# Performance work log

Hardware: AMD Instinct MI355X
Metric: run time of the kernel (lower is better)

Reference implementation:

```python
import jax, jax.numpy as jnp
import numpy as np

# Static problem configuration
NUM_GRAPHS = 64
NODES_PER_GRAPH = 2048          # divisible by OUT_H
NODE_EMB_DIM = 256              # divisible by OUT_W
COND_EMB_DIM = 64
OUT_H, OUT_W = 16, 8            # AdaptiveAvgPool2d output -> pooled dim H*W = 128
MLP_H = 256
BN_EPS = 1e-5


def setup_inputs() -> dict:
    key = jax.random.key(0)
    ks = jax.random.split(key, 8)
    N = NUM_GRAPHS * NODES_PER_GRAPH
    x = jax.random.normal(ks[0], (N, NODE_EMB_DIM), dtype=jnp.float32)
    # equal contiguous segments: node i belongs to graph i // NODES_PER_GRAPH
    batch = jnp.repeat(jnp.arange(NUM_GRAPHS, dtype=jnp.int64), NODES_PER_GRAPH)
    conditioner_z_ref = jax.random.normal(ks[1], (N, COND_EMB_DIM), dtype=jnp.float32)
    mlp_in = COND_EMB_DIM + OUT_H * OUT_W
    W1 = jax.random.normal(ks[2], (mlp_in, MLP_H), dtype=jnp.float32) / np.sqrt(mlp_in)
    b1 = jnp.zeros((MLP_H,), dtype=jnp.float32)
    gamma = jnp.ones((MLP_H,), dtype=jnp.float32)
    beta = jnp.zeros((MLP_H,), dtype=jnp.float32)
    W2 = jax.random.normal(ks[3], (MLP_H, 3), dtype=jnp.float32) / np.sqrt(MLP_H)
    b2 = jnp.zeros((3,), dtype=jnp.float32)
    return {"x": x, "batch": batch, "conditioner_z_ref": conditioner_z_ref,
            "W1": W1, "b1": b1, "gamma": gamma, "beta": beta, "W2": W2, "b2": b2}


def _adaptive_pool(x):
    # x: [N_total, D] with equal contiguous segments of NODES_PER_GRAPH rows per graph.
    # AdaptiveAvgPool2d((OUT_H, OUT_W)) on each [n, D] "image"; since n % OUT_H == 0
    # and D % OUT_W == 0 the adaptive bins are uniform -> exact reshape-mean.
    B = x.shape[0] // NODES_PER_GRAPH
    xg = x.reshape(B, OUT_H, NODES_PER_GRAPH // OUT_H, OUT_W, NODE_EMB_DIM // OUT_W)
    pooled = xg.mean(axis=(2, 4))                 # [B, OUT_H, OUT_W]
    return pooled.reshape(B, OUT_H * OUT_W)       # [B, H*W]


def reference(x, batch, conditioner_z_ref, W1, b1, gamma, beta, W2, b2):
    batch_pooled = _adaptive_pool(x)                          # [B, H*W]
    gathered = batch_pooled[batch]                            # [N, H*W]
    h = jnp.concatenate([conditioner_z_ref, gathered], axis=1)  # [N, cond + H*W]
    # Linear -> BatchNorm1d (training-mode batch stats, biased var) -> GELU (exact)
    h = h @ W1 + b1                                           # [N, MLP_H]
    mean = h.mean(axis=0)
    var = h.var(axis=0)
    h = (h - mean) * jax.lax.rsqrt(var + BN_EPS) * gamma + beta
    h = jax.nn.gelu(h, approximate=False)
    return h @ W2 + b2                                        # [N, 3]
```

## Files before the change

kernel.cpp:

```cpp
#include <hip/hip_runtime.h>
#include <math.h>

#define NG    64
#define NPG   2048
#define NTOT  (NG*NPG)
#define ZD    64
#define PD    128
#define MH    256

typedef __attribute__((ext_vector_type(8))) short bf16x8;
typedef __attribute__((ext_vector_type(4))) float f32x4;

__device__ __forceinline__ unsigned short f2bf(float f){
  unsigned u = __float_as_uint(f);
  unsigned r = u + 0x7FFFu + ((u >> 16) & 1u);
  return (unsigned short)(r >> 16);
}
__device__ __forceinline__ float bf2f(unsigned short s){
  return __uint_as_float(((unsigned)s) << 16);
}
__device__ __forceinline__ float gelu_f(float x){
  float u = x * x;
  float a = fmaf(0.044715f, u, 1.0f);
  float e = __builtin_amdgcn_exp2f(-2.3022083f * x * a);
  return x * __builtin_amdgcn_rcpf(1.0f + e);
}

__launch_bounds__(256)
__global__ void k1_pool_zstat(const float* __restrict__ x, const float* __restrict__ z,
                              float* __restrict__ pooled, float* __restrict__ St,
                              float* __restrict__ C){
  __shared__ __align__(16) unsigned short s_zt[64 * 264];
  __shared__ float s_cred[4096];
  int tid = threadIdx.x;

  if (blockIdx.x >= 256){
    int bi = blockIdx.x - 256;
    int b  = bi >> 4;
    int oh = bi & 15;
    int c4 = tid & 63;
    int rq = tid >> 6;
    const float4* x4 = (const float4*)x;
    size_t base = (size_t)(b * NPG + oh * 128) * 64;
    float4 acc = make_float4(0.f, 0.f, 0.f, 0.f);
    #pragma unroll 8
    for (int i = 0; i < 32; i++){
      float4 v = x4[base + (size_t)(rq + i * 4) * 64 + c4];
      acc.x += v.x; acc.y += v.y; acc.z += v.z; acc.w += v.w;
    }
    s_cred[tid] = acc.x + acc.y + acc.z + acc.w;
    __syncthreads();
    if (tid < 8){
      float s = 0.f;
      #pragma unroll
      for (int w = 0; w < 4; w++)
        #pragma unroll
        for (int j = 0; j < 8; j++)
          s += s_cred[w * 64 + tid * 8 + j];
      pooled[b * PD + oh * 8 + tid] = s * (1.0f / 4096.0f);
    }
    return;
  }

  int blk = blockIdx.x;
  int g = blk >> 2, q4 = blk & 3;
  int lane = tid & 63, wave = tid >> 6;
  int col = lane & 15, quad = lane >> 4;
  const float4* z4 = (const float4*)z + ((size_t)g * 2048 + q4 * 512) * 16;
  int d4 = col;
  int mg = quad;

  f32x4 acc[4][4];
  #pragma unroll
  for (int a = 0; a < 4; a++)
    #pragma unroll
    for (int b = 0; b < 4; b++) acc[a][b] = (f32x4)(0.f);
  float s0 = 0.f, s1 = 0.f, s2 = 0.f, s3 = 0.f;

  for (int ch = 0; ch < 2; ch++){
    #pragma unroll
    for (int rd = 0; rd < 4; rd++){
      int m0 = rd * 64 + wave * 16 + mg * 4;
      const float4* src = z4 + ch * 4096 + m0 * 16 + d4;
      float4 v0 = src[0];
      float4 v1 = src[16];
      float4 v2 = src[32];
      float4 v3 = src[48];
      s0 += v0.x + v1.x + v2.x + v3.x;
      s1 += v0.y + v1.y + v2.y + v3.y;
      s2 += v0.z + v1.z + v2.z + v3.z;
      s3 += v0.w + v1.w + v2.w + v3.w;
      int slot = m0 >> 3;
      int sub  = m0 & 4;
      int d0 = d4 * 4;
      {
        int d = d0 + 0; int ss = slot ^ ((d >> 3) & 7);
        ushort4 w = make_ushort4(f2bf(v0.x), f2bf(v1.x), f2bf(v2.x), f2bf(v3.x));
        *(ushort4*)&s_zt[d * 264 + ss * 8 + sub] = w;
      }
      {
        int d = d0 + 1; int ss = slot ^ ((d >> 3) & 7);
        ushort4 w = make_ushort4(f2bf(v0.y), f2bf(v1.y), f2bf(v2.y), f2bf(v3.y));
        *(ushort4*)&s_zt[d * 264 + ss * 8 + sub] = w;
      }
      {
        int d = d0 + 2; int ss = slot ^ ((d >> 3) & 7);
        ushort4 w = make_ushort4(f2bf(v0.z), f2bf(v1.z), f2bf(v2.z), f2bf(v3.z));
        *(ushort4*)&s_zt[d * 264 + ss * 8 + sub] = w;
      }
      {
        int d = d0 + 3; int ss = slot ^ ((d >> 3) & 7);
        ushort4 w = make_ushort4(f2bf(v0.w), f2bf(v1.w), f2bf(v2.w), f2bf(v3.w));
        *(ushort4*)&s_zt[d * 264 + ss * 8 + sub] = w;
      }
    }
    __syncthreads();
    #pragma unroll
    for (int ks = 0; ks < 2; ks++){
      bf16x8 fr[4];
      #pragma unroll
      for (int t = 0; t < 4; t++){
        int row = t * 16 + col;
        int ss  = (wave * 8 + ks * 4 + quad) ^ ((row >> 3) & 7);
        fr[t] = *(const bf16x8*)&s_zt[row * 264 + ss * 8];
      }
      #pragma unroll
      for (int mt = 0; mt < 4; mt++)
        #pragma unroll
        for (int nt = 0; nt < 4; nt++)
          acc[mt][nt] = __builtin_amdgcn_mfma_f32_16x16x32_bf16(fr[mt], fr[nt], acc[mt][nt], 0, 0, 0);
    }
    __syncthreads();
  }

  s0 += __shfl_xor(s0, 16); s0 += __shfl_xor(s0, 32);
  s1 += __shfl_xor(s1, 16); s1 += __shfl_xor(s1, 32);
  s2 += __shfl_xor(s2, 16); s2 += __shfl_xor(s2, 32);
  s3 += __shfl_xor(s3, 16); s3 += __shfl_xor(s3, 32);
  if (quad == 0){
    atomicAdd(&St[(d4 * 4 + 0) * 64 + g], s0);
    atomicAdd(&St[(d4 * 4 + 1) * 64 + g], s1);
    atomicAdd(&St[(d4 * 4 + 2) * 64 + g], s2);
    atomicAdd(&St[(d4 * 4 + 3) * 64 + g], s3);
  }

  #pragma unroll
  for (int w = 0; w < 4; w++){
    if (wave == w){
      #pragma unroll
      for (int mt = 0; mt < 4; mt++)
        #pragma unroll
        for (int nt = 0; nt < 4; nt++)
          #pragma unroll
          for (int r = 0; r < 4; r++){
            int p = mt * 16 + quad * 4 + r;
            int qc = nt * 16 + col;
            if (w == 0) s_cred[p * 64 + qc]  = acc[mt][nt][r];
            else        s_cred[p * 64 + qc] += acc[mt][nt][r];
          }
    }
    __syncthreads();
  }
  for (int f = tid; f < 4096; f += 256)
    atomicAdd(&C[f], s_cred[f]);
}

__launch_bounds__(256)
__global__ void k2_stats(const float* __restrict__ pooled, const float* __restrict__ W1,
                         const float* __restrict__ b1, const float* __restrict__ gamma,
                         const float* __restrict__ beta, const float* __restrict__ C,
                         const float* __restrict__ St, float* __restrict__ Aj,
                         float* __restrict__ cprime, unsigned short* __restrict__ Wbf){
  __shared__ float pl[64 * 129];
  int tid = threadIdx.x;
  int jc = tid >> 6, lane = tid & 63;
  int j = blockIdx.x * 4 + jc;

  Wbf[(size_t)j * 64 + lane] = f2bf(W1[(size_t)lane * 256 + j]);

  for (int idx = tid; idx < 8192; idx += 256)
    pl[(idx >> 7) * 129 + (idx & 127)] = pooled[idx];
  __syncthreads();

  float g = b1[j];
  #pragma unroll 8
  for (int k = 0; k < 128; k++)
    g = fmaf(pl[lane * 129 + k], W1[(size_t)(ZD + k) * MH + j], g);

  float wl = W1[(size_t)lane * MH + j];
  float t1 = 0.f, t2 = 0.f;
  #pragma unroll
  for (int q = 0; q < 64; q++){
    float wq = __uint_as_float(__builtin_amdgcn_readlane(__float_as_uint(wl), q));
    t1 = fmaf(C [q * 64 + lane], wq, t1);
    t2 = fmaf(St[q * 64 + lane], wq, t2);
  }
  float v_wcw = wl * t1;
  float v_gs  = g * t2;
  float v_s   = t2;
  float v_g   = g;
  float v_g2  = g * g;
  #pragma unroll
  for (int off = 32; off; off >>= 1){
    v_wcw += __shfl_xor(v_wcw, off);
    v_gs  += __shfl_xor(v_gs , off);
    v_s   += __shfl_xor(v_s  , off);
    v_g   += __shfl_xor(v_g  , off);
    v_g2  += __shfl_xor(v_g2 , off);
  }
  const float invN = 1.0f / (float)NTOT;
  float mean = v_s * invN + v_g * (1.0f / 64.0f);
  float eh2  = v_wcw * invN + 2.0f * invN * v_gs + v_g2 * (1.0f / 64.0f);
  float var  = eh2 - mean * mean;
  float aj = gamma[j] * rsqrtf(var + 1e-5f);
  if (lane == 0) Aj[j] = aj;
  cprime[lane * MH + j] = fmaf(aj, g, beta[j] - aj * mean);
}

__launch_bounds__(256, 4)
__global__ void final_kernel(const float* __restrict__ z, const unsigned short* __restrict__ Wbf,
                             const float* __restrict__ Aj, const float* __restrict__ cp,
                             const float* __restrict__ W2, const float* __restrict__ b2,
                             float* __restrict__ out){
  __shared__ __align__(16) unsigned short zt[64 * 136];
  __shared__ float slab[4 * 192];
  int tid = threadIdx.x;
  int u  = blockIdx.x;
  int n0 = u * 64;
  int g  = u >> 5;

  const float4* z4 = (const float4*)z + (size_t)n0 * 16;
  #pragma unroll
  for (int i = 0; i < 4; i++){
    int idx = tid + i * 256;
    int m = idx >> 4, d4 = idx & 15;
    float4 v = z4[idx];
    ushort4 h, l;
    h.x = f2bf(v.x); l.x = f2bf(v.x - bf2f(h.x));
    h.y = f2bf(v.y); l.y = f2bf(v.y - bf2f(h.y));
    h.z = f2bf(v.z); l.z = f2bf(v.z - bf2f(h.z));
    h.w = f2bf(v.w); l.w = f2bf(v.w - bf2f(h.w));
    *(ushort4*)&zt[m * 136 + d4 * 4]      = h;
    *(ushort4*)&zt[m * 136 + 64 + d4 * 4] = l;
  }
  __syncthreads();

  int lane = tid & 63, wave = tid >> 6;
  int col = lane & 15, quad = lane >> 4;
  int nbase = wave * 64;

  f32x4 acc[4][4];
  #pragma unroll
  for (int mt = 0; mt < 4; mt++)
    #pragma unroll
    for (int nt = 0; nt < 4; nt++) acc[mt][nt] = (f32x4)(0.f);

  #pragma unroll
  for (int ks = 0; ks < 4; ks++){
    int k0 = ks * 32;
    bf16x8 af[4];
    #pragma unroll
    for (int mt = 0; mt < 4; mt++)
      af[mt] = *(const bf16x8*)&zt[(mt * 16 + col) * 136 + k0 + quad * 8];
    #pragma unroll
    for (int nt = 0; nt < 4; nt++){
      bf16x8 bv = *(const bf16x8*)&Wbf[(size_t)(nbase + nt * 16 + col) * 64 + (ks & 1) * 32 + quad * 8];
      #pragma unroll
      for (int mt = 0; mt < 4; mt++)
        acc[mt][nt] = __builtin_amdgcn_mfma_f32_16x16x32_bf16(af[mt], bv, acc[mt][nt], 0, 0, 0);
    }
  }

  float aj[4], cj[4], w2a[4], w2b[4], w2c[4];
  #pragma unroll
  for (int nt = 0; nt < 4; nt++){
    int j = nbase + nt * 16 + col;
    aj[nt] = Aj[j];
    cj[nt] = cp[g * MH + j];
    w2a[nt] = W2[j * 3 + 0];
    w2b[nt] = W2[j * 3 + 1];
    w2c[nt] = W2[j * 3 + 2];
  }

  #pragma unroll
  for (int mt = 0; mt < 4; mt++){
    #pragma unroll
    for (int r = 0; r < 4; r++){
      float o0 = 0.f, o1 = 0.f, o2 = 0.f;
      #pragma unroll
      for (int nt = 0; nt < 4; nt++){
        float h  = fmaf(aj[nt], acc[mt][nt][r], cj[nt]);
        float ge = gelu_f(h);
        o0 = fmaf(ge, w2a[nt], o0);
        o1 = fmaf(ge, w2b[nt], o1);
        o2 = fmaf(ge, w2c[nt], o2);
      }
      #pragma unroll
      for (int off = 8; off; off >>= 1){
        o0 += __shfl_xor(o0, off);
        o1 += __shfl_xor(o1, off);
        o2 += __shfl_xor(o2, off);
      }
      if (col == 0){
        int node = mt * 16 + quad * 4 + r;
        slab[wave * 192 + node * 3 + 0] = o0;
        slab[wave * 192 + node * 3 + 1] = o1;
        slab[wave * 192 + node * 3 + 2] = o2;
      }
    }
  }
  __syncthreads();
  if (tid < 192){
    float b2v = b2[tid % 3];
    out[(size_t)u * 192 + tid] = slab[tid] + slab[192 + tid] + slab[384 + tid] + slab[576 + tid] + b2v;
  }
}

extern "C" void kernel_launch(void* const* d_in, const int* in_sizes, int n_in,
                              void* d_out, int out_size, void* d_ws, size_t ws_size,
                              hipStream_t stream){
  (void)in_sizes; (void)n_in; (void)out_size; (void)ws_size;
  const float* x     = (const float*)d_in[0];
  const float* z     = (const float*)d_in[2];
  const float* W1    = (const float*)d_in[3];
  const float* b1    = (const float*)d_in[4];
  const float* gamma = (const float*)d_in[5];
  const float* beta  = (const float*)d_in[6];
  const float* W2    = (const float*)d_in[7];
  const float* b2    = (const float*)d_in[8];
  float* out = (float*)d_out;

  float* W = (float*)d_ws;
  float* pooled = W;
  float* St     = W + 8192;
  float* C      = W + 12288;
  float* Aj     = W + 16384;
  float* CP     = W + 16640;
  unsigned short* Wbf = (unsigned short*)(W + 33024);

  hipMemsetAsync((char*)d_ws + 8192 * 4, 0, 8192 * 4, stream);

  k1_pool_zstat<<<dim3(1280), dim3(256), 0, stream>>>(x, z, pooled, St, C);
  k2_stats     <<<dim3(64),   dim3(256), 0, stream>>>(pooled, W1, b1, gamma, beta, C, St, Aj, CP, Wbf);
  final_kernel <<<dim3(NTOT / 64), dim3(256), 0, stream>>>(z, Wbf, Aj, CP, W2, b2, out);
}
```

Before: 270.8 us.

## Fuse three kernels into one persistent kernel with global atomic barriers

Replaces the three launches (pool/z-stats, BN stats, final MLP) with a single 512-block persistent kernel that separates phases with an atomic-counter grid barrier. Pooling work is redistributed so the stats blocks also do one pool tile and the others do three, and the final phase loops over node tiles. This is meant to remove launch gaps and tail effects between kernels. In exchange, correctness depends on all 512 blocks being co-resident, and occupancy is limited by the larger shared buffer and launch bounds of 2.

```diff
diff --git a/kernel.cpp b/kernel.cpp
--- a/kernel.cpp
+++ b/kernel.cpp
@@ -7,6 +7,7 @@
 #define ZD    64
 #define PD    128
 #define MH    256
+#define NBLK  512
 
 typedef __attribute__((ext_vector_type(8))) short bf16x8;
 typedef __attribute__((ext_vector_type(4))) float f32x4;
@@ -26,293 +27,310 @@
   return x * __builtin_amdgcn_rcpf(1.0f + e);
 }
 
-__launch_bounds__(256)
-__global__ void k1_pool_zstat(const float* __restrict__ x, const float* __restrict__ z,
-                              float* __restrict__ pooled, float* __restrict__ St,
-                              float* __restrict__ C){
-  __shared__ __align__(16) unsigned short s_zt[64 * 264];
-  __shared__ float s_cred[4096];
-  int tid = threadIdx.x;
-
-  if (blockIdx.x >= 256){
-    int bi = blockIdx.x - 256;
-    int b  = bi >> 4;
-    int oh = bi & 15;
-    int c4 = tid & 63;
-    int rq = tid >> 6;
-    const float4* x4 = (const float4*)x;
-    size_t base = (size_t)(b * NPG + oh * 128) * 64;
-    float4 acc = make_float4(0.f, 0.f, 0.f, 0.f);
-    #pragma unroll 8
-    for (int i = 0; i < 32; i++){
-      float4 v = x4[base + (size_t)(rq + i * 4) * 64 + c4];
-      acc.x += v.x; acc.y += v.y; acc.z += v.z; acc.w += v.w;
-    }
-    s_cred[tid] = acc.x + acc.y + acc.z + acc.w;
-    __syncthreads();
-    if (tid < 8){
-      float s = 0.f;
-      #pragma unroll
-      for (int w = 0; w < 4; w++)
-        #pragma unroll
-        for (int j = 0; j < 8; j++)
-          s += s_cred[w * 64 + tid * 8 + j];
-      pooled[b * PD + oh * 8 + tid] = s * (1.0f / 4096.0f);
-    }
-    return;
-  }
-
-  int blk = blockIdx.x;
-  int g = blk >> 2, q4 = blk & 3;
-  int lane = tid & 63, wave = tid >> 6;
-  int col = lane & 15, quad = lane >> 4;
-  const float4* z4 = (const float4*)z + ((size_t)g * 2048 + q4 * 512) * 16;
-  int d4 = col;
-  int mg = quad;
-
-  f32x4 acc[4][4];
-  #pragma unroll
-  for (int a = 0; a < 4; a++)
-    #pragma unroll
-    for (int b = 0; b < 4; b++) acc[a][b] = (f32x4)(0.f);
-  float s0 = 0.f, s1 = 0.f, s2 = 0.f, s3 = 0.f;
-
-  for (int ch = 0; ch < 2; ch++){
-    #pragma unroll
-    for (int rd = 0; rd < 4; rd++){
-      int m0 = rd * 64 + wave * 16 + mg * 4;
-      const float4* src = z4 + ch * 4096 + m0 * 16 + d4;
-      float4 v0 = src[0];
-      float4 v1 = src[16];
-      float4 v2 = src[32];
-      float4 v3 = src[48];
-      s0 += v0.x + v1.x + v2.x + v3.x;
-      s1 += v0.y + v1.y + v2.y + v3.y;
-      s2 += v0.z + v1.z + v2.z + v3.z;
-      s3 += v0.w + v1.w + v2.w + v3.w;
-      int slot = m0 >> 3;
-      int sub  = m0 & 4;
-      int d0 = d4 * 4;
-      {
-        int d = d0 + 0; int ss = slot ^ ((d >> 3) & 7);
-        ushort4 w = make_ushort4(f2bf(v0.x), f2bf(v1.x), f2bf(v2.x), f2bf(v3.x));
-        *(ushort4*)&s_zt[d * 264 + ss * 8 + sub] = w;
-      }
-      {
-        int d = d0 + 1; int ss = slot ^ ((d >> 3) & 7);
-        ushort4 w = make_ushort4(f2bf(v0.y), f2bf(v1.y), f2bf(v2.y), f2bf(v3.y));
-        *(ushort4*)&s_zt[d * 264 + ss * 8 + sub] = w;
-      }
-      {
-        int d = d0 + 2; int ss = slot ^ ((d >> 3) & 7);
-        ushort4 w = make_ushort4(f2bf(v0.z), f2bf(v1.z), f2bf(v2.z), f2bf(v3.z));
-        *(ushort4*)&s_zt[d * 264 + ss * 8 + sub] = w;
-      }
-      {
-        int d = d0 + 3; int ss = slot ^ ((d >> 3) & 7);
-        ushort4 w = make_ushort4(f2bf(v0.w), f2bf(v1.w), f2bf(v2.w), f2bf(v3.w));
-        *(ushort4*)&s_zt[d * 264 + ss * 8 + sub] = w;
-      }
-    }
-    __syncthreads();
-    #pragma unroll
-    for (int ks = 0; ks < 2; ks++){
-      bf16x8 fr[4];
-      #pragma unroll
-      for (int t = 0; t < 4; t++){
-        int row = t * 16 + col;
-        int ss  = (wave * 8 + ks * 4 + quad) ^ ((row >> 3) & 7);
-        fr[t] = *(const bf16x8*)&s_zt[row * 264 + ss * 8];
-      }
-      #pragma unroll
-      for (int mt = 0; mt < 4; mt++)
-        #pragma unroll
-        for (int nt = 0; nt < 4; nt++)
-          acc[mt][nt] = __builtin_amdgcn_mfma_f32_16x16x32_bf16(fr[mt], fr[nt], acc[mt][nt], 0, 0, 0);
-    }
-    __syncthreads();
-  }
-
-  s0 += __shfl_xor(s0, 16); s0 += __shfl_xor(s0, 32);
-  s1 += __shfl_xor(s1, 16); s1 += __shfl_xor(s1, 32);
-  s2 += __shfl_xor(s2, 16); s2 += __shfl_xor(s2, 32);
-  s3 += __shfl_xor(s3, 16); s3 += __shfl_xor(s3, 32);
-  if (quad == 0){
-    atomicAdd(&St[(d4 * 4 + 0) * 64 + g], s0);
-    atomicAdd(&St[(d4 * 4 + 1) * 64 + g], s1);
-    atomicAdd(&St[(d4 * 4 + 2) * 64 + g], s2);
-    atomicAdd(&St[(d4 * 4 + 3) * 64 + g], s3);
-  }
-
-  #pragma unroll
-  for (int w = 0; w < 4; w++){
-    if (wave == w){
-      #pragma unroll
-      for (int mt = 0; mt < 4; mt++)
-        #pragma unroll
-        for (int nt = 0; nt < 4; nt++)
-          #pragma unroll
-          for (int r = 0; r < 4; r++){
-            int p = mt * 16 + quad * 4 + r;
-            int qc = nt * 16 + col;
-            if (w == 0) s_cred[p * 64 + qc]  = acc[mt][nt][r];
-            else        s_cred[p * 64 + qc] += acc[mt][nt][r];
-          }
-    }
-    __syncthreads();
-  }
-  for (int f = tid; f < 4096; f += 256)
-    atomicAdd(&C[f], s_cred[f]);
-}
-
-__launch_bounds__(256)
-__global__ void k2_stats(const float* __restrict__ pooled, const float* __restrict__ W1,
-                         const float* __restrict__ b1, const float* __restrict__ gamma,
-                         const float* __restrict__ beta, const float* __restrict__ C,
-                         const float* __restrict__ St, float* __restrict__ Aj,
-                         float* __restrict__ cprime, unsigned short* __restrict__ Wbf){
-  __shared__ float pl[64 * 129];
-  int tid = threadIdx.x;
-  int jc = tid >> 6, lane = tid & 63;
-  int j = blockIdx.x * 4 + jc;
-
-  Wbf[(size_t)j * 64 + lane] = f2bf(W1[(size_t)lane * 256 + j]);
-
-  for (int idx = tid; idx < 8192; idx += 256)
-    pl[(idx >> 7) * 129 + (idx & 127)] = pooled[idx];
+__device__ __forceinline__ void gbar(int* bar, int target){
   __syncthreads();
-
-  float g = b1[j];
-  #pragma unroll 8
-  for (int k = 0; k < 128; k++)
-    g = fmaf(pl[lane * 129 + k], W1[(size_t)(ZD + k) * MH + j], g);
-
-  float wl = W1[(size_t)lane * MH + j];
-  float t1 = 0.f, t2 = 0.f;
-  #pragma unroll
-  for (int q = 0; q < 64; q++){
-    float wq = __uint_as_float(__builtin_amdgcn_readlane(__float_as_uint(wl), q));
-    t1 = fmaf(C [q * 64 + lane], wq, t1);
-    t2 = fmaf(St[q * 64 + lane], wq, t2);
-  }
-  float v_wcw = wl * t1;
-  float v_gs  = g * t2;
-  float v_s   = t2;
-  float v_g   = g;
-  float v_g2  = g * g;
-  #pragma unroll
-  for (int off = 32; off; off >>= 1){
-    v_wcw += __shfl_xor(v_wcw, off);
-    v_gs  += __shfl_xor(v_gs , off);
-    v_s   += __shfl_xor(v_s  , off);
-    v_g   += __shfl_xor(v_g  , off);
-    v_g2  += __shfl_xor(v_g2 , off);
-  }
-  const float invN = 1.0f / (float)NTOT;
-  float mean = v_s * invN + v_g * (1.0f / 64.0f);
-  float eh2  = v_wcw * invN + 2.0f * invN * v_gs + v_g2 * (1.0f / 64.0f);
-  float var  = eh2 - mean * mean;
-  float aj = gamma[j] * rsqrtf(var + 1e-5f);
-  if (lane == 0) Aj[j] = aj;
-  cprime[lane * MH + j] = fmaf(aj, g, beta[j] - aj * mean);
-}
-
-__launch_bounds__(256, 4)
-__global__ void final_kernel(const float* __restrict__ z, const unsigned short* __restrict__ Wbf,
-                             const float* __restrict__ Aj, const float* __restrict__ cp,
-                             const float* __restrict__ W2, const float* __restrict__ b2,
-                             float* __restrict__ out){
-  __shared__ __align__(16) unsigned short zt[64 * 136];
-  __shared__ float slab[4 * 192];
-  int tid = threadIdx.x;
-  int u  = blockIdx.x;
-  int n0 = u * 64;
-  int g  = u >> 5;
-
-  const float4* z4 = (const float4*)z + (size_t)n0 * 16;
-  #pragma unroll
-  for (int i = 0; i < 4; i++){
-    int idx = tid + i * 256;
-    int m = idx >> 4, d4 = idx & 15;
-    float4 v = z4[idx];
-    ushort4 h, l;
-    h.x = f2bf(v.x); l.x = f2bf(v.x - bf2f(h.x));
-    h.y = f2bf(v.y); l.y = f2bf(v.y - bf2f(h.y));
-    h.z = f2bf(v.z); l.z = f2bf(v.z - bf2f(h.z));
-    h.w = f2bf(v.w); l.w = f2bf(v.w - bf2f(h.w));
-    *(ushort4*)&zt[m * 136 + d4 * 4]      = h;
-    *(ushort4*)&zt[m * 136 + 64 + d4 * 4] = l;
+  if (threadIdx.x == 0){
+    __threadfence();
+    atomicAdd(bar, 1);
+    while (__hip_atomic_load(bar, __ATOMIC_RELAXED, __HIP_MEMORY_SCOPE_AGENT) < target)
+      __builtin_amdgcn_s_sleep(2);
+    __threadfence();
   }
   __syncthreads();
-
-  int lane = tid & 63, wave = tid >> 6;
-  int col = lane & 15, quad = lane >> 4;
-  int nbase = wave * 64;
-
-  f32x4 acc[4][4];
-  #pragma unroll
-  for (int mt = 0; mt < 4; mt++)
+}
+
+__launch_bounds__(256, 2)
+__global__ void mega(const float* __restrict__ x, const float* __restrict__ z,
+                     const float* __restrict__ W1, const float* __restrict__ b1,
+                     const float* __restrict__ gamma, const float* __restrict__ beta,
+                     const float* __restrict__ W2, const float* __restrict__ b2,
+                     float* __restrict__ pooled, float* __restrict__ St,
+                     float* __restrict__ C, float* __restrict__ Aj,
+                     float* __restrict__ cp, unsigned short* __restrict__ Wbf,
+                     float* __restrict__ out, int* __restrict__ bar){
+  __shared__ __align__(16) unsigned char smem[50176];
+  int tid = threadIdx.x;
+  int bid = blockIdx.x;
+
+  {
+    unsigned short* s_zt = (unsigned short*)smem;
+    float* s_cred = (float*)(smem + 33792);
+
+    if (bid < 256){
+      int g = bid >> 2, q4 = bid & 3;
+      int lane = tid & 63, wave = tid >> 6;
+      int col = lane & 15, quad = lane >> 4;
+      const float4* z4 = (const float4*)z + ((size_t)g * 2048 + q4 * 512) * 16;
+      int d4 = col;
+      int mg = quad;
+
+      f32x4 acc[4][4];
+      #pragma unroll
+      for (int a = 0; a < 4; a++)
+        #pragma unroll
+        for (int b = 0; b < 4; b++) acc[a][b] = (f32x4)(0.f);
+      float s0 = 0.f, s1 = 0.f, s2 = 0.f, s3 = 0.f;
+
+      for (int ch = 0; ch < 2; ch++){
+        #pragma unroll
+        for (int rd = 0; rd < 4; rd++){
+          int m0 = rd * 64 + wave * 16 + mg * 4;
+          const float4* src = z4 + ch * 4096 + m0 * 16 + d4;
+          float4 v0 = src[0];
+          float4 v1 = src[16];
+          float4 v2 = src[32];
+          float4 v3 = src[48];
+          s0 += v0.x + v1.x + v2.x + v3.x;
+          s1 += v0.y + v1.y + v2.y + v3.y;
+          s2 += v0.z + v1.z + v2.z + v3.z;
+          s3 += v0.w + v1.w + v2.w + v3.w;
+          int slot = m0 >> 3;
+          int sub  = m0 & 4;
+          int d0 = d4 * 4;
+          {
+            int d = d0 + 0; int ss = slot ^ ((d >> 3) & 7);
+            ushort4 w = make_ushort4(f2bf(v0.x), f2bf(v1.x), f2bf(v2.x), f2bf(v3.x));
+            *(ushort4*)&s_zt[d * 264 + ss * 8 + sub] = w;
+          }
+          {
+            int d = d0 + 1; int ss = slot ^ ((d >> 3) & 7);
+            ushort4 w = make_ushort4(f2bf(v0.y), f2bf(v1.y), f2bf(v2.y), f2bf(v3.y));
+            *(ushort4*)&s_zt[d * 264 + ss * 8 + sub] = w;
+          }
+          {
+            int d = d0 + 2; int ss = slot ^ ((d >> 3) & 7);
+            ushort4 w = make_ushort4(f2bf(v0.z), f2bf(v1.z), f2bf(v2.z), f2bf(v3.z));
+            *(ushort4*)&s_zt[d * 264 + ss * 8 + sub] = w;
+          }
+          {
+            int d = d0 + 3; int ss = slot ^ ((d >> 3) & 7);
+            ushort4 w = make_ushort4(f2bf(v0.w), f2bf(v1.w), f2bf(v2.w), f2bf(v3.w));
+            *(ushort4*)&s_zt[d * 264 + ss * 8 + sub] = w;
+          }
+        }
+        __syncthreads();
+        #pragma unroll
+        for (int ks = 0; ks < 2; ks++){
+          bf16x8 fr[4];
+          #pragma unroll
+          for (int t = 0; t < 4; t++){
+            int row = t * 16 + col;
+            int ss  = (wave * 8 + ks * 4 + quad) ^ ((row >> 3) & 7);
+            fr[t] = *(const bf16x8*)&s_zt[row * 264 + ss * 8];
+          }
+          #pragma unroll
+          for (int mt = 0; mt < 4; mt++)
+            #pragma unroll
+            for (int nt = 0; nt < 4; nt++)
+              acc[mt][nt] = __builtin_amdgcn_mfma_f32_16x16x32_bf16(fr[mt], fr[nt], acc[mt][nt], 0, 0, 0);
+        }
+        __syncthreads();
+      }
+
+      s0 += __shfl_xor(s0, 16); s0 += __shfl_xor(s0, 32);
+      s1 += __shfl_xor(s1, 16); s1 += __shfl_xor(s1, 32);
+      s2 += __shfl_xor(s2, 16); s2 += __shfl_xor(s2, 32);
+      s3 += __shfl_xor(s3, 16); s3 += __shfl_xor(s3, 32);
+      if (quad == 0){
+        atomicAdd(&St[(d4 * 4 + 0) * 64 + g], s0);
+        atomicAdd(&St[(d4 * 4 + 1) * 64 + g], s1);
+        atomicAdd(&St[(d4 * 4 + 2) * 64 + g], s2);
+        atomicAdd(&St[(d4 * 4 + 3) * 64 + g], s3);
+      }
+
+      #pragma unroll
+      for (int w = 0; w < 4; w++){
+        if (wave == w){
+          #pragma unroll
+          for (int mt = 0; mt < 4; mt++)
+            #pragma unroll
+            for (int nt = 0; nt < 4; nt++)
+              #pragma unroll
+              for (int r = 0; r < 4; r++){
+                int p = mt * 16 + quad * 4 + r;
+                int qc = nt * 16 + col;
+                if (w == 0) s_cred[p * 64 + qc]  = acc[mt][nt][r];
+                else        s_cred[p * 64 + qc] += acc[mt][nt][r];
+              }
+        }
+        __syncthreads();
+      }
+      for (int f = tid; f < 4096; f += 256)
+        atomicAdd(&C[f], s_cred[f]);
+    }
+
+    int u0 = bid, nu = (bid < 256) ? 1 : 3;
+    for (int k = 0; k < nu; k++){
+      int bi = u0 + k * 256;
+      int b  = bi >> 4;
+      int oh = bi & 15;
+      int c4 = tid & 63;
+      int rq = tid >> 6;
+      const float4* x4 = (const float4*)x;
+      size_t base = (size_t)(b * NPG + oh * 128) * 64;
+      float4 acc = make_float4(0.f, 0.f, 0.f, 0.f);
+      #pragma unroll 8
+      for (int i = 0; i < 32; i++){
+        float4 v = x4[base + (size_t)(rq + i * 4) * 64 + c4];
+        acc.x += v.x; acc.y += v.y; acc.z += v.z; acc.w += v.w;
+      }
+      __syncthreads();
+      s_cred[tid] = acc.x + acc.y + acc.z + acc.w;
+      __syncthreads();
+      if (tid < 8){
+        float s = 0.f;
+        #pragma unroll
+        for (int w = 0; w < 4; w++)
+          #pragma unroll
+          for (int j = 0; j < 8; j++)
+            s += s_cred[w * 64 + tid * 8 + j];
+        pooled[b * PD + oh * 8 + tid] = s * (1.0f / 4096.0f);
+      }
+    }
+  }
+  gbar(bar, NBLK);
+
+  if (bid < 64){
+    float* pl = (float*)smem;
+    int jc = tid >> 6, lane = tid & 63;
+    int j = bid * 4 + jc;
+
+    Wbf[(size_t)j * 64 + lane] = f2bf(W1[(size_t)lane * 256 + j]);
+
+    for (int idx = tid; idx < 8192; idx += 256)
+      pl[(idx >> 7) * 129 + (idx & 127)] = pooled[idx];
+    __syncthreads();
+
+    float g = b1[j];
+    #pragma unroll 8
+    for (int k = 0; k < 128; k++)
+      g = fmaf(pl[lane * 129 + k], W1[(size_t)(ZD + k) * MH + j], g);
+
+    float wl = W1[(size_t)lane * MH + j];
+    float t1 = 0.f, t2 = 0.f;
     #pragma unroll
-    for (int nt = 0; nt < 4; nt++) acc[mt][nt] = (f32x4)(0.f);
-
-  #pragma unroll
-  for (int ks = 0; ks < 4; ks++){
-    int k0 = ks * 32;
-    bf16x8 af[4];
+    for (int q = 0; q < 64; q++){
+      float wq = __uint_as_float(__builtin_amdgcn_readlane(__float_as_uint(wl), q));
+      t1 = fmaf(C [q * 64 + lane], wq, t1);
+      t2 = fmaf(St[q * 64 + lane], wq, t2);
+    }
+    float v_wcw = wl * t1;
+    float v_gs  = g * t2;
+    float v_s   = t2;
+    float v_g   = g;
+    float v_g2  = g * g;
     #pragma unroll
-    for (int mt = 0; mt < 4; mt++)
-      af[mt] = *(const bf16x8*)&zt[(mt * 16 + col) * 136 + k0 + quad * 8];
-    #pragma unroll
-    for (int nt = 0; nt < 4; nt++){
-      bf16x8 bv = *(const bf16x8*)&Wbf[(size_t)(nbase + nt * 16 + col) * 64 + (ks & 1) * 32 + quad * 8];
+    for (int off = 32; off; off >>= 1){
+      v_wcw += __shfl_xor(v_wcw, off);
+      v_gs  += __shfl_xor(v_gs , off);
+      v_s   += __shfl_xor(v_s  , off);
+      v_g   += __shfl_xor(v_g  , off);
+      v_g2  += __shfl_xor(v_g2 , off);
+    }
+    const float invN = 1.0f / (float)NTOT;
+    float mean = v_s * invN + v_g * (1.0f / 64.0f);
+    float eh2  = v_wcw * invN + 2.0f * invN * v_gs + v_g2 * (1.0f / 64.0f);
+    float var  = eh2 - mean * mean;
+    float aj = gamma[j] * rsqrtf(var + 1e-5f);
+    if (lane == 0) Aj[j] = aj;
+    cp[lane * MH + j] = fmaf(aj, g, beta[j] - aj * mean);
+  }
+  gbar(bar, 2 * NBLK);
+
+  {
+    unsigned short* zt = (unsigned short*)smem;
+    float* slab = (float*)(smem + 17408);
+    int lane = tid & 63, wave = tid >> 6;
+    int col = lane & 15, quad = lane >> 4;
+    int nbase = wave * 64;
+
+    for (int u = bid; u < 2048; u += NBLK){
+      int n0 = u * 64;
+      int g  = u >> 5;
+
+      const float4* z4 = (const float4*)z + (size_t)n0 * 16;
+      #pragma unroll
+      for (int i = 0; i < 4; i++){
+        int idx = tid + i * 256;
+        int m = idx >> 4, d4 = idx & 15;
+        float4 v = z4[idx];
+        ushort4 h, l;
+        h.x = f2bf(v.x); l.x = f2bf(v.x - bf2f(h.x));
+        h.y = f2bf(v.y); l.y = f2bf(v.y - bf2f(h.y));
+        h.z = f2bf(v.z); l.z = f2bf(v.z - bf2f(h.z));
+        h.w = f2bf(v.w); l.w = f2bf(v.w - bf2f(h.w));
+        *(ushort4*)&zt[m * 136 + d4 * 4]      = h;
+        *(ushort4*)&zt[m * 136 + 64 + d4 * 4] = l;
+      }
+      __syncthreads();
+
+      f32x4 acc[4][4];
       #pragma unroll
       for (int mt = 0; mt < 4; mt++)
-        acc[mt][nt] = __builtin_amdgcn_mfma_f32_16x16x32_bf16(af[mt], bv, acc[mt][nt], 0, 0, 0);
-    }
-  }
-
-  float aj[4], cj[4], w2a[4], w2b[4], w2c[4];
-  #pragma unroll
-  for (int nt = 0; nt < 4; nt++){
-    int j = nbase + nt * 16 + col;
-    aj[nt] = Aj[j];
-    cj[nt] = cp[g * MH + j];
-    w2a[nt] = W2[j * 3 + 0];
-    w2b[nt] = W2[j * 3 + 1];
-    w2c[nt] = W2[j * 3 + 2];
-  }
-
-  #pragma unroll
-  for (int mt = 0; mt < 4; mt++){
-    #pragma unroll
-    for (int r = 0; r < 4; r++){
-      float o0 = 0.f, o1 = 0.f, o2 = 0.f;
+        #pragma unroll
+        for (int nt = 0; nt < 4; nt++) acc[mt][nt] = (f32x4)(0.f);
+
+      #pragma unroll
+      for (int ks = 0; ks < 4; ks++){
+        int k0 = ks * 32;
+        bf16x8 af[4];
+        #pragma unroll
+        for (int mt = 0; mt < 4; mt++)
+          af[mt] = *(const bf16x8*)&zt[(mt * 16 + col) * 136 + k0 + quad * 8];
+        #pragma unroll
+        for (int nt = 0; nt < 4; nt++){
+          bf16x8 bv = *(const bf16x8*)&Wbf[(size_t)(nbase + nt * 16 + col) * 64 + (ks & 1) * 32 + quad * 8];
+          #pragma unroll
+          for (int mt = 0; mt < 4; mt++)
+            acc[mt][nt] = __builtin_amdgcn_mfma_f32_16x16x32_bf16(af[mt], bv, acc[mt][nt], 0, 0, 0);
+        }
+      }
+
+      float aj[4], cj[4], w2a[4], w2b[4], w2c[4];
       #pragma unroll
       for (int nt = 0; nt < 4; nt++){
-        float h  = fmaf(aj[nt], acc[mt][nt][r], cj[nt]);
-        float ge = gelu_f(h);
-        o0 = fmaf(ge, w2a[nt], o0);
-        o1 = fmaf(ge, w2b[nt], o1);
-        o2 = fmaf(ge, w2c[nt], o2);
-      }
-      #pragma unroll
-      for (int off = 8; off; off >>= 1){
-        o0 += __shfl_xor(o0, off);
-        o1 += __shfl_xor(o1, off);
-        o2 += __shfl_xor(o2, off);
-      }
-      if (col == 0){
-        int node = mt * 16 + quad * 4 + r;
-        slab[wave * 192 + node * 3 + 0] = o0;
-        slab[wave * 192 + node * 3 + 1] = o1;
-        slab[wave * 192 + node * 3 + 2] = o2;
-      }
-    }
-  }
-  __syncthreads();
-  if (tid < 192){
-    float b2v = b2[tid % 3];
-    out[(size_t)u * 192 + tid] = slab[tid] + slab[192 + tid] + slab[384 + tid] + slab[576 + tid] + b2v;
+        int j = nbase + nt * 16 + col;
+        aj[nt] = Aj[j];
+        cj[nt] = cp[g * MH + j];
+        w2a[nt] = W2[j * 3 + 0];
+        w2b[nt] = W2[j * 3 + 1];
+        w2c[nt] = W2[j * 3 + 2];
+      }
+
+      #pragma unroll
+      for (int mt = 0; mt < 4; mt++){
+        #pragma unroll
+        for (int r = 0; r < 4; r++){
+          float o0 = 0.f, o1 = 0.f, o2 = 0.f;
+          #pragma unroll
+          for (int nt = 0; nt < 4; nt++){
+            float h  = fmaf(aj[nt], acc[mt][nt][r], cj[nt]);
+            float ge = gelu_f(h);
+            o0 = fmaf(ge, w2a[nt], o0);
+            o1 = fmaf(ge, w2b[nt], o1);
+            o2 = fmaf(ge, w2c[nt], o2);
+          }
+          #pragma unroll
+          for (int off = 8; off; off >>= 1){
+            o0 += __shfl_xor(o0, off);
+            o1 += __shfl_xor(o1, off);
+            o2 += __shfl_xor(o2, off);
+          }
+          if (col == 0){
+            int node = mt * 16 + quad * 4 + r;
+            slab[wave * 192 + node * 3 + 0] = o0;
+            slab[wave * 192 + node * 3 + 1] = o1;
+            slab[wave * 192 + node * 3 + 2] = o2;
+          }
+        }
+      }
+      __syncthreads();
+      if (tid < 192){
+        float b2v = b2[tid % 3];
+        out[(size_t)u * 192 + tid] = slab[tid] + slab[192 + tid] + slab[384 + tid] + slab[576 + tid] + b2v;
+      }
+      __syncthreads();
+    }
   }
 }
 
@@ -334,13 +352,13 @@
   float* pooled = W;
   float* St     = W + 8192;
   float* C      = W + 12288;
-  float* Aj     = W + 16384;
-  float* CP     = W + 16640;
-  unsigned short* Wbf = (unsigned short*)(W + 33024);
-
-  hipMemsetAsync((char*)d_ws + 8192 * 4, 0, 8192 * 4, stream);
-
-  k1_pool_zstat<<<dim3(1280), dim3(256), 0, stream>>>(x, z, pooled, St, C);
-  k2_stats     <<<dim3(64),   dim3(256), 0, stream>>>(pooled, W1, b1, gamma, beta, C, St, Aj, CP, Wbf);
-  final_kernel <<<dim3(NTOT / 64), dim3(256), 0, stream>>>(z, Wbf, Aj, CP, W2, b2, out);
-}
+  int*   bar    = (int*)(W + 16384);
+  float* Aj     = W + 16448;
+  float* CP     = W + 16704;
+  unsigned short* Wbf = (unsigned short*)(W + 33088);
+
+  hipMemsetAsync((char*)d_ws + 8192 * 4, 0, (4096 + 4096 + 64) * 4, stream);
+
+  mega<<<dim3(NBLK), dim3(256), 0, stream>>>(x, z, W1, b1, gamma, beta, W2, b2,
+                                             pooled, St, C, Aj, CP, Wbf, out, bar);
+}
```

New measurement: 368.8 us. 36.2% more time.
